# Kernel tuning notes

Measured on AMD Instinct MI355X. Metric: run time of the kernel, lower is better.

Reference implementation:

```python
import jax, jax.numpy as jnp
import numpy as np
import math

B, N, D, H = 32, 512, 512, 8
DK = D // H
MAX_DIST = 100.0
BINS = 20
BIN_SIZE = MAX_DIST / BINS


def setup_inputs() -> dict:
    key = jax.random.key(0)
    ks = jax.random.split(key, 12)
    s = 1.0 / math.sqrt(D)
    inp = {
        "x": jax.random.normal(ks[0], (B, N, D), dtype=jnp.float32),
        "distance_matrix": jax.random.uniform(ks[1], (B, N, N), dtype=jnp.float32) * MAX_DIST,
        "Wq": jax.random.uniform(ks[2], (D, D), jnp.float32, -s, s),
        "bq": jax.random.uniform(ks[3], (D,), jnp.float32, -s, s),
        "Wk": jax.random.uniform(ks[4], (D, D), jnp.float32, -s, s),
        "bk": jax.random.uniform(ks[5], (D,), jnp.float32, -s, s),
        "Wv": jax.random.uniform(ks[6], (D, D), jnp.float32, -s, s),
        "bv": jax.random.uniform(ks[7], (D,), jnp.float32, -s, s),
        "Wo": jax.random.uniform(ks[8], (D, D), jnp.float32, -s, s),
        "bo": jax.random.uniform(ks[9], (D,), jnp.float32, -s, s),
        "dist_weights": jnp.ones((BINS + 1,), dtype=jnp.float32),
    }
    return inp


def reference(x, distance_matrix, Wq, bq, Wk, bk, Wv, bv, Wo, bo, dist_weights):
    temperature = 1.0
    # Linear projections; torch nn.Linear computes x @ W.T + b
    q = (x @ Wq.T + bq).reshape(B, N, H, DK).transpose(0, 2, 1, 3)  # [B,H,N,DK]
    k = (x @ Wk.T + bk).reshape(B, N, H, DK).transpose(0, 2, 1, 3)
    v = (x @ Wv.T + bv).reshape(B, N, H, DK).transpose(0, 2, 1, 3)

    scores = jnp.einsum("bhqd,bhkd->bhqk", q, k) / math.sqrt(DK)  # [B,H,N,N]

    # Relative position bias: bin distances, look up scalar weight per pair
    binned = jnp.clip((distance_matrix / BIN_SIZE).astype(jnp.int32), 0, BINS)  # [B,N,N]
    bias = dist_weights[binned] / temperature  # [B,N,N]
    scores = scores + bias[:, None, :, :]  # broadcast over heads

    attn = jax.nn.softmax(scores, axis=-1)  # dropout is identity in eval
    out = jnp.einsum("bhqk,bhkd->bhqd", attn, v)  # [B,H,N,DK]
    out = out.transpose(0, 2, 1, 3).reshape(B, N, D)
    return out @ Wo.T + bo
```

## Files before the change

### kernel.cpp

```cpp
#include <hip/hip_runtime.h>
#include <hip/hip_fp16.h>
#include <math.h>
#include <stdint.h>

#define BB 32
#define NN 512
#define DDIM 512
#define HH 8
#define DK 64

typedef __attribute__((ext_vector_type(8))) short short8;
typedef __attribute__((ext_vector_type(8))) _Float16 half8;
typedef __attribute__((ext_vector_type(4))) float floatx4;
typedef __attribute__((ext_vector_type(16))) float floatx16;
typedef unsigned short ushort_t;
typedef unsigned int uint_t;

__device__ __forceinline__ void gl_lds16(const void* g, void* l) {
    __builtin_amdgcn_global_load_lds(
        (const __attribute__((address_space(1))) uint_t*)g,
        (__attribute__((address_space(3))) uint_t*)l,
        16, 0, 0);
}

__device__ __forceinline__ ushort_t f2bf(float f) {
    uint_t u = __builtin_bit_cast(uint_t, f);
    u += 0x7fff + ((u >> 16) & 1);
    return (ushort_t)(u >> 16);
}

__device__ __forceinline__ uint_t pkbf(float a, float b) {
    return (uint_t)f2bf(a) | ((uint_t)f2bf(b) << 16);
}

__device__ __forceinline__ uint_t pkh(float a, float b) {
    return __builtin_bit_cast(uint_t, __builtin_amdgcn_cvt_pkrtz(a, b));
}

__device__ __forceinline__ float h2f(ushort_t u) {
    return __half2float(__ushort_as_half(u));
}

__global__ __launch_bounds__(256) void prep_all(
    const float* __restrict__ x, const float* __restrict__ dist,
    const float* __restrict__ dw,
    const float* __restrict__ Wq, const float* __restrict__ Wk,
    const float* __restrict__ Wv, const float* __restrict__ Wo,
    ushort_t* __restrict__ xb, ushort_t* __restrict__ Tm,
    ushort_t* __restrict__ wqb, ushort_t* __restrict__ wkb,
    ushort_t* __restrict__ wvb, ushort_t* __restrict__ wob) {
    const int bx = blockIdx.x;
    if (bx < 4096) {
        const int i = bx * 256 + threadIdx.x;
        const float4 a = ((const float4*)x)[i * 2 + 0];
        const float4 b = ((const float4*)x)[i * 2 + 1];
        uint4 o;
        o.x = pkbf(a.x, a.y); o.y = pkbf(a.z, a.w);
        o.z = pkbf(b.x, b.y); o.w = pkbf(b.z, b.w);
        *(uint4*)(xb + (size_t)i * 8) = o;
    } else if (bx < 8192) {
        __shared__ float dws[21];
        if (threadIdx.x < 21) dws[threadIdx.x] = (dw[threadIdx.x] - 3.0f) * 1.44269504f;
        __syncthreads();
        const int i = (bx - 4096) * 256 + threadIdx.x;
        float dv[8];
        { const float4 a = ((const float4*)dist)[i * 2 + 0];
          const float4 b = ((const float4*)dist)[i * 2 + 1];
          dv[0]=a.x; dv[1]=a.y; dv[2]=a.z; dv[3]=a.w;
          dv[4]=b.x; dv[5]=b.y; dv[6]=b.z; dv[7]=b.w; }
        ushort_t h[8];
        #pragma unroll
        for (int j = 0; j < 8; ++j) {
            int bin = (int)(dv[j] / 5.0f);
            bin = bin < 0 ? 0 : (bin > 20 ? 20 : bin);
            h[j] = __half_as_ushort(__float2half(dws[bin]));
        }
        uint4 o;
        o.x = (uint_t)h[0] | ((uint_t)h[1] << 16);
        o.y = (uint_t)h[2] | ((uint_t)h[3] << 16);
        o.z = (uint_t)h[4] | ((uint_t)h[5] << 16);
        o.w = (uint_t)h[6] | ((uint_t)h[7] << 16);
        *(uint4*)(Tm + (size_t)i * 8) = o;
    } else {
        const int bw = bx - 8192;
        const int w = bw >> 7;
        const float* s; ushort_t* d;
        if (w == 0)      { s = Wq; d = wqb; }
        else if (w == 1) { s = Wk; d = wkb; }
        else if (w == 2) { s = Wv; d = wvb; }
        else             { s = Wo; d = wob; }
        const int i = (bw & 127) * 256 + threadIdx.x;
        const float4 a = ((const float4*)s)[i * 2 + 0];
        const float4 b = ((const float4*)s)[i * 2 + 1];
        uint4 o;
        o.x = pkbf(a.x, a.y); o.y = pkbf(a.z, a.w);
        o.z = pkbf(b.x, b.y); o.w = pkbf(b.z, b.w);
        *(uint4*)(d + (size_t)i * 8) = o;
    }
}

#define GEMM_CORE(Aptr, Wptr, M0, N0)                                                   \
    __shared__ ushort_t SH[2][128 * 32];                                                \
    ushort_t* const As = SH[0];                                                         \
    ushort_t* const Bs = SH[1];                                                         \
    const int tid = threadIdx.x;                                                        \
    const int lane = tid & 63, wid = tid >> 6;                                          \
    const int quad = lane >> 4, l15 = lane & 15;                                        \
    const int m0 = (M0), n0 = (N0);                                                     \
    const int wy = wid >> 1, wx = wid & 1;                                              \
    floatx4 acc[4][4];                                                                  \
    _Pragma("unroll") for (int i = 0; i < 4; ++i)                                       \
        _Pragma("unroll") for (int j = 0; j < 4; ++j)                                   \
            _Pragma("unroll") for (int r = 0; r < 4; ++r) acc[i][j][r] = 0.f;           \
    for (int k0 = 0; k0 < DDIM; k0 += 32) {                                             \
        __syncthreads();                                                                \
        _Pragma("unroll") for (int j = 0; j < 4; ++j) {                                 \
            const int t = wid * 4 + j;                                                  \
            const int rowi = ((t & 7) << 4) + (lane >> 2);                              \
            const int cd = (lane & 3) ^ ((rowi >> 1) & 3);                              \
            if (t < 8)                                                                  \
                gl_lds16(Aptr + (size_t)(m0 + rowi) * DDIM + k0 + cd * 8,               \
                         (char*)As + ((t & 7) << 10));                                  \
            else                                                                        \
                gl_lds16(Wptr + (size_t)(n0 + rowi) * DDIM + k0 + cd * 8,               \
                         (char*)Bs + ((t & 7) << 10));                                  \
        }                                                                               \
        __syncthreads();                                                                \
        short8 aw[4], bt[4];                                                            \
        _Pragma("unroll") for (int fi = 0; fi < 4; ++fi) {                              \
            const int r = wy * 64 + fi * 16 + l15;                                      \
            aw[fi] = *(const short8*)((const char*)Bs + r * 64 +                        \
                                      ((quad ^ ((r >> 1) & 3)) << 4));                  \
        }                                                                               \
        _Pragma("unroll") for (int ti = 0; ti < 4; ++ti) {                              \
            const int r = wx * 64 + ti * 16 + l15;                                      \
            bt[ti] = *(const short8*)((const char*)As + r * 64 +                        \
                                      ((quad ^ ((r >> 1) & 3)) << 4));                  \
        }                                                                               \
        _Pragma("unroll") for (int fi = 0; fi < 4; ++fi)                                \
            _Pragma("unroll") for (int ti = 0; ti < 4; ++ti)                            \
                acc[fi][ti] = __builtin_amdgcn_mfma_f32_16x16x32_bf16(                  \
                    aw[fi], bt[ti], acc[fi][ti], 0, 0, 0);                              \
    }

__global__ __launch_bounds__(256) void gemm_qkv(
    const ushort_t* __restrict__ A,
    const ushort_t* __restrict__ W0, const ushort_t* __restrict__ W1,
    const ushort_t* __restrict__ W2,
    const float* __restrict__ b0, const float* __restrict__ b1,
    const float* __restrict__ b2,
    ushort_t* __restrict__ o0, ushort_t* __restrict__ o1, ushort_t* __restrict__ o2) {
    const ushort_t* W; const float* bias; ushort_t* dst;
    if (blockIdx.z == 0)      { W = W0; bias = b0; dst = o0; }
    else if (blockIdx.z == 1) { W = W1; bias = b1; dst = o1; }
    else                      { W = W2; bias = b2; dst = o2; }
    const bool as_f16 = (blockIdx.z == 2);
    GEMM_CORE(A, W, blockIdx.x * 128, blockIdx.y * 128)
    if (as_f16) {
        const int b = m0 >> 9;
        const int hh0 = n0 >> 6;
        ushort_t* const SHT = &SH[0][0];
        __syncthreads();
        #pragma unroll
        for (int hp = 0; hp < 2; ++hp) {
            if (wy == hp) {
                #pragma unroll
                for (int fi = 0; fi < 4; ++fi) {
                    const int f = n0 + wy * 64 + fi * 16 + quad * 4;
                    const float4 b4 = *(const float4*)&bias[f];
                    #pragma unroll
                    for (int ti = 0; ti < 4; ++ti) {
                        const int q = wx * 64 + ti * 16 + l15;
                        const int qc = q >> 3, qr = q & 7;
                        const float vv[4] = {acc[fi][ti][0] + b4.x,
                                             acc[fi][ti][1] + b4.y,
                                             acc[fi][ti][2] + b4.z,
                                             acc[fi][ti][3] + b4.w};
                        #pragma unroll
                        for (int r = 0; r < 4; ++r) {
                            const int d = fi * 16 + quad * 4 + r;
                            SHT[(d * 256 + ((qc ^ (d & 15)) << 4) + qr * 2) >> 1] =
                                __half_as_ushort(__float2half(vv[r]));
                        }
                    }
                }
            }
            __syncthreads();
            const size_t vbase = ((size_t)(b * HH + hh0 + hp)) * DK;
            #pragma unroll
            for (int c = 0; c < 4; ++c) {
                const int ch = tid + 256 * c;
                const int d = ch >> 4, chl = ch & 15;
                const uint4 vv = *(const uint4*)((const char*)SHT + d * 256 +
                                                 ((chl ^ (d & 15)) << 4));
                *(uint4*)&dst[(vbase + d) * NN + (m0 & 511) + chl * 8] = vv;
            }
            __syncthreads();
        }
    } else {
        #pragma unroll
        for (int fi = 0; fi < 4; ++fi) {
            const int f = n0 + wy * 64 + fi * 16 + quad * 4;
            const float4 b4 = *(const float4*)&bias[f];
            #pragma unroll
            for (int ti = 0; ti < 4; ++ti) {
                const int token = m0 + wx * 64 + ti * 16 + l15;
                const float v0 = acc[fi][ti][0] + b4.x, v1 = acc[fi][ti][1] + b4.y;
                const float v2 = acc[fi][ti][2] + b4.z, v3 = acc[fi][ti][3] + b4.w;
                uint2 v;
                v.x = pkbf(v0, v1); v.y = pkbf(v2, v3);
                *(uint2*)&dst[(size_t)token * DDIM + f] = v;
            }
        }
    }
}

__global__ __launch_bounds__(256) void gemm_out(
    const ushort_t* __restrict__ A, const ushort_t* __restrict__ Wo,
    const float* __restrict__ bo, float* __restrict__ dst) {
    GEMM_CORE(A, Wo, blockIdx.x * 128, blockIdx.y * 128)
    #pragma unroll
    for (int fi = 0; fi < 4; ++fi) {
        const int f = n0 + wy * 64 + fi * 16 + quad * 4;
        const float4 b4 = *(const float4*)&bo[f];
        #pragma unroll
        for (int ti = 0; ti < 4; ++ti) {
            const int token = m0 + wx * 64 + ti * 16 + l15;
            float4 v;
            v.x = acc[fi][ti][0] + b4.x; v.y = acc[fi][ti][1] + b4.y;
            v.z = acc[fi][ti][2] + b4.z; v.w = acc[fi][ti][3] + b4.w;
            *(float4*)&dst[(size_t)token * DDIM + f] = v;
        }
    }
}

__global__ __launch_bounds__(512)
__attribute__((amdgpu_waves_per_eu(2, 2)))
void attn_fused(
    const ushort_t* __restrict__ Qg, const ushort_t* __restrict__ Kg,
    const ushort_t* __restrict__ Vtg, const ushort_t* __restrict__ Tg,
    ushort_t* __restrict__ aout) {
    __shared__ ushort_t Ks[512 * 64];
    __shared__ ushort_t Vs[64 * 512];

    const int tid = threadIdx.x, lane = tid & 63, wid = tid >> 6;
    const int l31 = lane & 31, hl = lane >> 5;
    const int p = blockIdx.x;
    const int nid = (p & 7) * 32 + (p >> 3);
    const int h = nid & 7, b = nid >> 3;
    const float K1 = 0.18033688f;

    #pragma unroll
    for (int j = 0; j < 8; ++j) {
        const int t = wid * 8 + j;
        {
            const int row = t * 8 + (lane >> 3);
            const int key = (row & 7) ^ ((row >> 3) & 7);
            const int g = (lane & 7) ^ key;
            gl_lds16(Kg + (size_t)(b * NN + row) * DDIM + h * DK + g * 8,
                     (char*)Ks + t * 1024);
        }
        {
            const int key = (t & 7) ^ ((t >> 3) & 7);
            const int g = lane ^ key;
            gl_lds16(Vtg + (size_t)((b * HH + h) * DK + t) * NN + g * 8,
                     (char*)Vs + t * 1024);
        }
    }

    short8 bq[2][4];
    #pragma unroll
    for (int qt = 0; qt < 2; ++qt) {
        const ushort_t* qp =
            Qg + (size_t)(b * NN + wid * 64 + qt * 32 + l31) * DDIM + h * DK + hl * 8;
        #pragma unroll
        for (int st = 0; st < 4; ++st) bq[qt][st] = *(const short8*)(qp + st * 16);
    }

    float lsum[2] = {0.f, 0.f};
    floatx16 O[2][2];
    #pragma unroll
    for (int qt = 0; qt < 2; ++qt)
        #pragma unroll
        for (int dt = 0; dt < 2; ++dt)
            #pragma unroll
            for (int r = 0; r < 16; ++r) O[qt][dt][r] = 0.f;

    __syncthreads();

    for (int kt = 0; kt < 8; ++kt) {
        uint2 tv[2][2][4];
        #pragma unroll
        for (int qt = 0; qt < 2; ++qt) {
            const ushort_t* tp =
                Tg + (size_t)(b * NN + wid * 64 + qt * 32 + l31) * NN + kt * 64 + hl * 4;
            #pragma unroll
            for (int kti = 0; kti < 2; ++kti)
                #pragma unroll
                for (int g = 0; g < 4; ++g)
                    tv[qt][kti][g] = *(const uint2*)(tp + kti * 32 + g * 8);
        }

        #pragma unroll
        for (int kti = 0; kti < 2; ++kti) {
            short8 kf[4];
            {
                const int row = kt * 64 + kti * 32 + l31;
                const int key = (row & 7) ^ ((row >> 3) & 7);
                #pragma unroll
                for (int st = 0; st < 4; ++st)
                    kf[st] = *(const short8*)((const char*)Ks + row * 128 +
                                              (((st * 2 + hl) ^ key) << 4));
            }
            half8 vf[2][2];
            #pragma unroll
            for (int dt = 0; dt < 2; ++dt) {
                const int d = dt * 32 + l31;
                const int key = (d & 7) ^ ((d >> 3) & 7);
                #pragma unroll
                for (int ks = 0; ks < 2; ++ks)
                    vf[dt][ks] = *(const half8*)((const char*)Vs + d * 1024 +
                        (((kt * 8 + kti * 4 + ks * 2 + hl) ^ key) << 4));
            }

            #pragma unroll
            for (int qt = 0; qt < 2; ++qt) {
                floatx16 S;
                #pragma unroll
                for (int r = 0; r < 16; ++r) S[r] = 0.f;
                __builtin_amdgcn_s_setprio(1);
                #pragma unroll
                for (int st = 0; st < 4; ++st)
                    S = __builtin_amdgcn_mfma_f32_32x32x16_bf16(
                        kf[st], bq[qt][st], S, 0, 0, 0);
                __builtin_amdgcn_s_setprio(0);

                float ls = 0.f;
                #pragma unroll
                for (int ks = 0; ks < 2; ++ks) {
                    float pp[8];
                    #pragma unroll
                    for (int gg = 0; gg < 2; ++gg) {
                        const uint2 tg = tv[qt][kti][ks * 2 + gg];
                        const float t0 = h2f((ushort_t)tg.x);
                        const float t1 = h2f((ushort_t)(tg.x >> 16));
                        const float t2 = h2f((ushort_t)tg.y);
                        const float t3 = h2f((ushort_t)(tg.y >> 16));
                        const int sb = ks * 8 + gg * 4;
                        pp[gg * 4 + 0] = exp2f(S[sb + 0] * K1 + t0);
                        pp[gg * 4 + 1] = exp2f(S[sb + 1] * K1 + t1);
                        pp[gg * 4 + 2] = exp2f(S[sb + 2] * K1 + t2);
                        pp[gg * 4 + 3] = exp2f(S[sb + 3] * K1 + t3);
                        ls += (pp[gg * 4 + 0] + pp[gg * 4 + 1]) +
                              (pp[gg * 4 + 2] + pp[gg * 4 + 3]);
                    }
                    uint_t w0 = pkh(pp[0], pp[1]);
                    uint_t w1 = pkh(pp[2], pp[3]);
                    uint_t w2 = pkh(pp[4], pp[5]);
                    uint_t w3 = pkh(pp[6], pp[7]);
                    auto r02 = __builtin_amdgcn_permlane32_swap(w0, w2, false, false);
                    auto r13 = __builtin_amdgcn_permlane32_swap(w1, w3, false, false);
                    uint4 uu;
                    uu.x = r02[0];
                    uu.y = r13[0];
                    uu.z = r02[1];
                    uu.w = r13[1];
                    const half8 bp = __builtin_bit_cast(half8, uu);

                    __builtin_amdgcn_s_setprio(1);
                    #pragma unroll
                    for (int dt = 0; dt < 2; ++dt)
                        O[qt][dt] = __builtin_amdgcn_mfma_f32_32x32x16_f16(
                            vf[dt][ks], bp, O[qt][dt], 0, 0, 0);
                    __builtin_amdgcn_s_setprio(0);
                }
                lsum[qt] += ls;
            }
        }
    }

    #pragma unroll
    for (int qt = 0; qt < 2; ++qt) {
        float l = lsum[qt];
        l += __shfl_xor(l, 32);
        const float inv = 1.0f / l;
        const size_t orow =
            (size_t)(b * NN + wid * 64 + qt * 32 + l31) * DDIM + h * DK;
        #pragma unroll
        for (int dt = 0; dt < 2; ++dt)
            #pragma unroll
            for (int g = 0; g < 4; ++g) {
                const int d = dt * 32 + g * 8 + hl * 4;
                uint2 ov;
                ov.x = pkbf(O[qt][dt][g * 4 + 0] * inv, O[qt][dt][g * 4 + 1] * inv);
                ov.y = pkbf(O[qt][dt][g * 4 + 2] * inv, O[qt][dt][g * 4 + 3] * inv);
                *(uint2*)&aout[orow + d] = ov;
            }
    }
}

extern "C" void kernel_launch(void* const* d_in, const int* in_sizes, int n_in,
                              void* d_out, int out_size, void* d_ws, size_t ws_size,
                              hipStream_t stream) {
    const float* x    = (const float*)d_in[0];
    const float* dist = (const float*)d_in[1];
    const float* Wq   = (const float*)d_in[2];
    const float* bq   = (const float*)d_in[3];
    const float* Wk   = (const float*)d_in[4];
    const float* bk   = (const float*)d_in[5];
    const float* Wv   = (const float*)d_in[6];
    const float* bv   = (const float*)d_in[7];
    const float* Wo   = (const float*)d_in[8];
    const float* bo   = (const float*)d_in[9];
    const float* dw   = (const float*)d_in[10];
    float* out = (float*)d_out;

    const size_t NELT = (size_t)BB * NN * DDIM;
    ushort_t* xb  = (ushort_t*)d_ws;
    ushort_t* wqb = xb + NELT;
    ushort_t* wkb = wqb + DDIM * DDIM;
    ushort_t* wvb = wkb + DDIM * DDIM;
    ushort_t* wob = wvb + DDIM * DDIM;
    ushort_t* qb  = wob + DDIM * DDIM;
    ushort_t* kb  = qb + NELT;
    ushort_t* vt  = kb + NELT;
    ushort_t* Tm  = vt + NELT;
    ushort_t* ab  = xb;

    prep_all<<<8704, 256, 0, stream>>>(x, dist, dw, Wq, Wk, Wv, Wo,
                                       xb, Tm, wqb, wkb, wvb, wob);
    gemm_qkv<<<dim3(128, 4, 3), 256, 0, stream>>>(xb, wqb, wkb, wvb, bq, bk, bv,
                                                  qb, kb, vt);
    attn_fused<<<256, 512, 0, stream>>>(qb, kb, vt, Tm, ab);
    gemm_out<<<dim3(128, 4), 256, 0, stream>>>(ab, wob, bo, out);
}
```

Baseline: 228.5 us.

## Fuse Q, K, V projections into one block sharing the staged x tile

The QKV GEMM now computes all three projections in each block. The x tile is loaded into LDS once per k-step and reused against the Wq, Wk and Wv tiles, instead of launching three separate grid slices that each reload x. This cuts global and LDS traffic for the activation, but it triples the accumulator registers per thread (48 floatx4) and reduces the grid from 1536 to 512 blocks. Occupancy is pinned to 2 waves per EU, and only one wave issues staging loads for each operand.

```diff
diff --git a/kernel.cpp b/kernel.cpp
--- a/kernel.cpp
+++ b/kernel.cpp
@@ -143,20 +143,92 @@
                     aw[fi], bt[ti], acc[fi][ti], 0, 0, 0);                              \
     }
 
-__global__ __launch_bounds__(256) void gemm_qkv(
+__global__ __launch_bounds__(256)
+__attribute__((amdgpu_waves_per_eu(2, 2)))
+void gemm_qkv(
     const ushort_t* __restrict__ A,
     const ushort_t* __restrict__ W0, const ushort_t* __restrict__ W1,
     const ushort_t* __restrict__ W2,
     const float* __restrict__ b0, const float* __restrict__ b1,
     const float* __restrict__ b2,
     ushort_t* __restrict__ o0, ushort_t* __restrict__ o1, ushort_t* __restrict__ o2) {
-    const ushort_t* W; const float* bias; ushort_t* dst;
-    if (blockIdx.z == 0)      { W = W0; bias = b0; dst = o0; }
-    else if (blockIdx.z == 1) { W = W1; bias = b1; dst = o1; }
-    else                      { W = W2; bias = b2; dst = o2; }
-    const bool as_f16 = (blockIdx.z == 2);
-    GEMM_CORE(A, W, blockIdx.x * 128, blockIdx.y * 128)
-    if (as_f16) {
+    __shared__ ushort_t SH[4][128 * 32];
+    const int tid = threadIdx.x;
+    const int lane = tid & 63, wid = tid >> 6;
+    const int quad = lane >> 4, l15 = lane & 15;
+    const int m0 = blockIdx.x * 128, n0 = blockIdx.y * 128;
+    const int wy = wid >> 1, wx = wid & 1;
+
+    floatx4 acc[3][4][4];
+    #pragma unroll
+    for (int w = 0; w < 3; ++w)
+        #pragma unroll
+        for (int i = 0; i < 4; ++i)
+            #pragma unroll
+            for (int j = 0; j < 4; ++j)
+                #pragma unroll
+                for (int r = 0; r < 4; ++r) acc[w][i][j][r] = 0.f;
+
+    const ushort_t* const stage_src =
+        (wid == 0) ? A : (wid == 1 ? W0 : (wid == 2 ? W1 : W2));
+    const int stage_base = (wid == 0) ? m0 : n0;
+
+    for (int k0 = 0; k0 < DDIM; k0 += 32) {
+        __syncthreads();
+        #pragma unroll
+        for (int j = 0; j < 8; ++j) {
+            const int rowi = (j << 4) + (lane >> 2);
+            const int cd = (lane & 3) ^ ((rowi >> 1) & 3);
+            gl_lds16(stage_src + (size_t)(stage_base + rowi) * DDIM + k0 + cd * 8,
+                     (char*)&SH[wid][0] + (j << 10));
+        }
+        __syncthreads();
+        short8 bt[4];
+        #pragma unroll
+        for (int ti = 0; ti < 4; ++ti) {
+            const int r = wx * 64 + ti * 16 + l15;
+            bt[ti] = *(const short8*)((const char*)&SH[0][0] + r * 64 +
+                                      ((quad ^ ((r >> 1) & 3)) << 4));
+        }
+        #pragma unroll
+        for (int w = 0; w < 3; ++w) {
+            short8 aw[4];
+            #pragma unroll
+            for (int fi = 0; fi < 4; ++fi) {
+                const int r = wy * 64 + fi * 16 + l15;
+                aw[fi] = *(const short8*)((const char*)&SH[1 + w][0] + r * 64 +
+                                          ((quad ^ ((r >> 1) & 3)) << 4));
+            }
+            #pragma unroll
+            for (int fi = 0; fi < 4; ++fi)
+                #pragma unroll
+                for (int ti = 0; ti < 4; ++ti)
+                    acc[w][fi][ti] = __builtin_amdgcn_mfma_f32_16x16x32_bf16(
+                        aw[fi], bt[ti], acc[w][fi][ti], 0, 0, 0);
+        }
+    }
+
+    #pragma unroll
+    for (int w = 0; w < 2; ++w) {
+        const float* const bias = w ? b1 : b0;
+        ushort_t* const dst = w ? o1 : o0;
+        #pragma unroll
+        for (int fi = 0; fi < 4; ++fi) {
+            const int f = n0 + wy * 64 + fi * 16 + quad * 4;
+            const float4 b4 = *(const float4*)&bias[f];
+            #pragma unroll
+            for (int ti = 0; ti < 4; ++ti) {
+                const int token = m0 + wx * 64 + ti * 16 + l15;
+                const float v0 = acc[w][fi][ti][0] + b4.x, v1 = acc[w][fi][ti][1] + b4.y;
+                const float v2 = acc[w][fi][ti][2] + b4.z, v3 = acc[w][fi][ti][3] + b4.w;
+                uint2 v;
+                v.x = pkbf(v0, v1); v.y = pkbf(v2, v3);
+                *(uint2*)&dst[(size_t)token * DDIM + f] = v;
+            }
+        }
+    }
+
+    {
         const int b = m0 >> 9;
         const int hh0 = n0 >> 6;
         ushort_t* const SHT = &SH[0][0];
@@ -167,15 +239,15 @@
                 #pragma unroll
                 for (int fi = 0; fi < 4; ++fi) {
                     const int f = n0 + wy * 64 + fi * 16 + quad * 4;
-                    const float4 b4 = *(const float4*)&bias[f];
+                    const float4 b4 = *(const float4*)&b2[f];
                     #pragma unroll
                     for (int ti = 0; ti < 4; ++ti) {
                         const int q = wx * 64 + ti * 16 + l15;
                         const int qc = q >> 3, qr = q & 7;
-                        const float vv[4] = {acc[fi][ti][0] + b4.x,
-                                             acc[fi][ti][1] + b4.y,
-                                             acc[fi][ti][2] + b4.z,
-                                             acc[fi][ti][3] + b4.w};
+                        const float vv[4] = {acc[2][fi][ti][0] + b4.x,
+                                             acc[2][fi][ti][1] + b4.y,
+                                             acc[2][fi][ti][2] + b4.z,
+                                             acc[2][fi][ti][3] + b4.w};
                         #pragma unroll
                         for (int r = 0; r < 4; ++r) {
                             const int d = fi * 16 + quad * 4 + r;
@@ -193,24 +265,9 @@
                 const int d = ch >> 4, chl = ch & 15;
                 const uint4 vv = *(const uint4*)((const char*)SHT + d * 256 +
                                                  ((chl ^ (d & 15)) << 4));
-                *(uint4*)&dst[(vbase + d) * NN + (m0 & 511) + chl * 8] = vv;
+                *(uint4*)&o2[(vbase + d) * NN + (m0 & 511) + chl * 8] = vv;
             }
             __syncthreads();
-        }
-    } else {
-        #pragma unroll
-        for (int fi = 0; fi < 4; ++fi) {
-            const int f = n0 + wy * 64 + fi * 16 + quad * 4;
-            const float4 b4 = *(const float4*)&bias[f];
-            #pragma unroll
-            for (int ti = 0; ti < 4; ++ti) {
-                const int token = m0 + wx * 64 + ti * 16 + l15;
-                const float v0 = acc[fi][ti][0] + b4.x, v1 = acc[fi][ti][1] + b4.y;
-                const float v2 = acc[fi][ti][2] + b4.z, v3 = acc[fi][ti][3] + b4.w;
-                uint2 v;
-                v.x = pkbf(v0, v1); v.y = pkbf(v2, v3);
-                *(uint2*)&dst[(size_t)token * DDIM + f] = v;
-            }
         }
     }
 }
@@ -429,8 +486,8 @@
 
     prep_all<<<8704, 256, 0, stream>>>(x, dist, dw, Wq, Wk, Wv, Wo,
                                        xb, Tm, wqb, wkb, wvb, wob);
-    gemm_qkv<<<dim3(128, 4, 3), 256, 0, stream>>>(xb, wqb, wkb, wvb, bq, bk, bv,
-                                                  qb, kb, vt);
+    gemm_qkv<<<dim3(128, 4), 256, 0, stream>>>(xb, wqb, wkb, wvb, bq, bk, bv,
+                                               qb, kb, vt);
     attn_fused<<<256, 512, 0, stream>>>(qb, kb, vt, Tm, ab);
     gemm_out<<<dim3(128, 4), 256, 0, stream>>>(ab, wob, bo, out);
 }
```

New measurement: 224.9 us. About the same (-1.6%).
